# Optimization experiments

Measured on AMD Instinct MI355X. Metric: run time of the kernel, lower is better.

## Reference

```python
import jax, jax.numpy as jnp
import numpy as np

B, T, H, NPRED = 256, 512, 512, 128


def setup_inputs() -> dict:
    key = jax.random.key(0)
    ks = jax.random.split(key, 16)
    s = 1.0 / np.sqrt(H)
    u = lambda k, shape: jax.random.uniform(k, shape, jnp.float32, -s, s)
    return {
        "x": jax.random.normal(ks[0], (B, T), jnp.float32),
        # PyTorch LSTM params, gate order (i, f, g, o); bias = b_ih + b_hh fused
        "enc_Wih0": u(ks[1], (4 * H, 1)),
        "enc_Whh0": u(ks[2], (4 * H, H)),
        "enc_b0": u(ks[3], (4 * H,)),
        "enc_Wih1": u(ks[4], (4 * H, H)),
        "enc_Whh1": u(ks[5], (4 * H, H)),
        "enc_b1": u(ks[6], (4 * H,)),
        "dec_Wih0": u(ks[7], (4 * H, 1)),
        "dec_Whh0": u(ks[8], (4 * H, H)),
        "dec_b0": u(ks[9], (4 * H,)),
        "dec_Wih1": u(ks[10], (4 * H, H)),
        "dec_Whh1": u(ks[11], (4 * H, H)),
        "dec_b1": u(ks[12], (4 * H,)),
        "lin_W": u(ks[13], (H,)),
        "lin_b": u(ks[14], ()),
        "num_predictions": NPRED,
    }


def _cell(xp, h, c, Whh):
    # xp: x @ Wih.T + b (precomputed), shape [B, 4H]
    g = xp + h @ Whh.T
    i, f, gg, o = jnp.split(g, 4, axis=-1)
    c2 = jax.nn.sigmoid(f) * c + jax.nn.sigmoid(i) * jnp.tanh(gg)
    h2 = jax.nn.sigmoid(o) * jnp.tanh(c2)
    return h2, c2


def _lstm_layer(xs, Wih, Whh, b):
    # xs: [B, T, D] -> outputs [B, T, H], final (h, c) each [B, H]
    xp = jnp.einsum('btd,gd->btg', xs, Wih) + b  # input projection for all steps
    Bb = xs.shape[0]
    h0 = jnp.zeros((Bb, Whh.shape[1]), xs.dtype)
    c0 = jnp.zeros_like(h0)

    def step(carry, xt):
        h, c = carry
        h2, c2 = _cell(xt, h, c, Whh)
        return (h2, c2), h2

    (hT, cT), hs = jax.lax.scan(step, (h0, c0), jnp.swapaxes(xp, 0, 1))
    return jnp.swapaxes(hs, 0, 1), hT, cT


def reference(x, enc_Wih0, enc_Whh0, enc_b0, enc_Wih1, enc_Whh1, enc_b1,
              dec_Wih0, dec_Whh0, dec_b0, dec_Wih1, dec_Whh1, dec_b1,
              lin_W, lin_b, num_predictions):
    # Encoder: 2-layer LSTM over the full sequence (encode() feeds [B,T,1] once)
    h_l0, e_h0, e_c0 = _lstm_layer(x[:, :, None], enc_Wih0, enc_Whh0, enc_b0)
    _, e_h1, e_c1 = _lstm_layer(h_l0, enc_Wih1, enc_Whh1, enc_b1)

    def dec_step(carry, _):
        h0, c0, h1, c1, prev = carry
        xp0 = prev[:, None] @ dec_Wih0.T + dec_b0  # [B, 4H]
        h0n, c0n = _cell(xp0, h0, c0, dec_Whh0)
        xp1 = h0n @ dec_Wih1.T + dec_b1
        h1n, c1n = _cell(xp1, h1, c1, dec_Whh1)
        pred = h1n @ lin_W + lin_b  # [B]
        return (h0n, c0n, h1n, c1n, pred), pred

    carry0 = (e_h0, e_c0, e_h1, e_c1, x[:, -1])
    _, preds = jax.lax.scan(dec_step, carry0, None, length=num_predictions)
    return jnp.swapaxes(preds, 0, 1)  # [B, num_predictions]
```

## Files before the change

### kernel.cpp

```cpp
#include <hip/hip_runtime.h>

#define Hh 512
#define Bb 256
#define Tt 512
#define NPR 128
#define BH (Bb*Hh)
#define WN (4*Hh*Hh)
#define LDSB (131072 + 256)

typedef __attribute__((ext_vector_type(8))) short bf8;
typedef __attribute__((ext_vector_type(4))) float f4;
typedef __attribute__((ext_vector_type(4))) unsigned u4;

#define MF(A,B,C) C = __builtin_amdgcn_mfma_f32_16x16x32_bf16(A,B,C,0,0,0)
#define ALD(p)    __hip_atomic_load((p),  __ATOMIC_RELAXED, __HIP_MEMORY_SCOPE_AGENT)
#define AST(p,v)  __hip_atomic_store((p), (v), __ATOMIC_RELAXED, __HIP_MEMORY_SCOPE_AGENT)

__device__ __forceinline__ void ld16(u4& d, const u4* p) {
  asm volatile("global_load_dwordx4 %0, %1, off sc0 sc1" : "=&v"(d) : "v"(p));
}
__device__ __forceinline__ void st16(u4* p, u4 d) {
  asm volatile("global_store_dwordx4 %0, %1, off sc0 sc1" :: "v"(p), "v"(d) : "memory");
}
__device__ __forceinline__ bf8 asbf8(u4 v) {
  union { u4 u; bf8 b; } c; c.u = v; return c.b;
}
#define VW16 { asm volatile("s_waitcnt vmcnt(16)" ::: "memory"); __builtin_amdgcn_sched_barrier(0); }
#define VW0  { asm volatile("s_waitcnt vmcnt(0)"  ::: "memory"); __builtin_amdgcn_sched_barrier(0); }

__device__ __forceinline__ unsigned short f2bf(float x) {
  unsigned u = __float_as_uint(x);
  return (unsigned short)((u + 0x7FFFu + ((u >> 16) & 1u)) >> 16);
}
__device__ __forceinline__ float bf2f(unsigned short h) {
  return __uint_as_float((unsigned)h << 16);
}

__device__ __forceinline__ float sigm(float x) {
  return __builtin_amdgcn_rcpf(1.f + __expf(-x));
}
__device__ __forceinline__ float tanh_f(float x) {
  x = fminf(15.f, fmaxf(-15.f, x));
  const float e = __expf(2.f * x);
  return (e - 1.f) * __builtin_amdgcn_rcpf(e + 1.f);
}

__device__ __forceinline__ u4 pack8(unsigned short v, int lane) {
  unsigned x = v;
  unsigned p1 = (unsigned)__shfl_xor((int)x, 1, 64);
  unsigned u  = (lane & 1) ? ((p1 & 0xFFFFu) | (x << 16)) : ((x & 0xFFFFu) | (p1 << 16));
  unsigned p2 = (unsigned)__shfl_xor((int)u, 2, 64);
  unsigned d0 = (lane & 2) ? p2 : u;
  unsigned d1 = (lane & 2) ? u  : p2;
  unsigned q0 = (unsigned)__shfl_xor((int)d0, 4, 64);
  unsigned q1 = (unsigned)__shfl_xor((int)d1, 4, 64);
  u4 r;
  if (lane & 4) { r[0] = q0; r[1] = q1; r[2] = d0; r[3] = d1; }
  else          { r[0] = d0; r[1] = d1; r[2] = q0; r[3] = q1; }
  return r;
}

struct KP {
  const float *x, *eb0, *eb1, *db0, *db1, *eWih0, *dWih0, *linW, *linb;
  const unsigned short *eWhh0h,*eWhh0l,*eWih1h,*eWih1l,*eWhh1h,*eWhh1l;
  const unsigned short *dWhh0h,*dWhh0l,*dWih1h,*dWih1l,*dWhh1h,*dWhh1l;
  u4 *h0h0,*h0h1,*h0l0,*h0l1,*h1h0,*h1h1,*h1l0,*h1l1;
  float *c0,*c1,*pred,*out;
  unsigned *bar;
};

__device__ void gsync(unsigned* bar, unsigned rnd) {
  asm volatile("s_waitcnt vmcnt(0)" ::: "memory");
  __syncthreads();
  if (threadIdx.x == 0) {
    const int grp = blockIdx.x >> 4;
    unsigned* garr  = bar + grp*32;
    unsigned* cctr  = bar + 512;
    unsigned* cflag = bar + 576;
    const unsigned a = __hip_atomic_fetch_add(garr, 1u, __ATOMIC_RELAXED, __HIP_MEMORY_SCOPE_AGENT);
    if (a == rnd*16u + 15u) {
      const unsigned r = __hip_atomic_fetch_add(cctr, 1u, __ATOMIC_RELAXED, __HIP_MEMORY_SCOPE_AGENT);
      if (r == rnd*16u + 15u) AST(cflag, rnd + 1u);
    }
    while (ALD(cflag) <= rnd) __builtin_amdgcn_s_sleep(2);
  }
  __syncthreads();
  asm volatile("" ::: "memory");
}

__device__ void stageA_w(const unsigned short* Wh, const unsigned short* Wl, int j0, char* L) {
  const int t = threadIdx.x;
  const int r = t >> 2, q = t & 3;
  const int n = (r >> 4)*Hh + j0 + (r & 15);
  const unsigned short* gh = Wh + (size_t)n*Hh;
  const unsigned short* gl = Wl + (size_t)n*Hh;
  char* rowp = L + r*1024;
  #pragma unroll
  for (int u = 0; u < 16; ++u) {
    const int s = q*16 + u;
    const int so = (s ^ (r & 7)) * 16;
    *(uint4*)(rowp + so)         = *(const uint4*)(gh + s*8);
    *(uint4*)(rowp + 65536 + so) = *(const uint4*)(gl + s*8);
  }
  __syncthreads();
}
__device__ void stageB_w(const unsigned short* Wh, const unsigned short* Wl, int j0, char* slab) {
  const int t = threadIdx.x;
  const int r = t >> 3, q = t & 7;
  const int n = (r >> 3)*Hh + j0 + (r & 7);
  const unsigned short* gh = Wh + (size_t)n*Hh;
  const unsigned short* gl = Wl + (size_t)n*Hh;
  char* rowp = slab + r*1024;
  #pragma unroll
  for (int u = 0; u < 8; ++u) {
    const int s = q*8 + u;
    const int so = (s ^ (r & 7)) * 16;
    *(uint4*)(rowp + so)         = *(const uint4*)(gh + s*8);
    *(uint4*)(rowp + 32768 + so) = *(const uint4*)(gl + s*8);
  }
  __syncthreads();
}

__device__ __forceinline__ void stepA(const KP& kp, const char* L, float* sS,
    int m0, int j0, int jg,
    const u4* Ah, const u4* Al,
    const float* sW, const float* bias, float* cst,
    u4* Ho, u4* Lo,
    int smode, int sarg)
{
  const int tid = threadIdx.x;
  if (smode == 0) {
    if (tid < 64) sS[tid] = kp.x[(size_t)(m0 + tid)*Tt + sarg];
  } else {
    const int bl = tid >> 2, part = tid & 3;
    const int b = m0 + bl;
    float a = 0.f;
    #pragma unroll
    for (int u = 0; u < 16; ++u)
      a += ALD(&kp.pred[(part*16 + u)*Bb + b]);
    a += __shfl_xor(a, 1, 64);
    a += __shfl_xor(a, 2, 64);
    const float s = a + kp.linb[0];
    if (part == 0) {
      sS[bl] = s;
      if (jg == 0 && sarg >= 1) kp.out[(size_t)b*NPR + (sarg - 1)] = s;
    }
  }
  __syncthreads();

  const int wv = tid >> 6, lane = tid & 63;
  const int r15 = lane & 15, kg = lane >> 4;
  const int bb = m0 + wv*16 + r15;
  const u4* pAh = Ah + kg*256 + bb;
  const u4* pAl = Al + kg*256 + bb;
  f4 acc[4];
  #pragma unroll
  for (int g = 0; g < 4; ++g) acc[g] = (f4){0.f,0.f,0.f,0.f};
  const int swz = r15 & 7;

  u4 vh[16], vl[16];
  #pragma unroll
  for (int q = 0; q < 16; ++q) {
    ld16(vh[q], pAh + q*1024);
    ld16(vl[q], pAl + q*1024);
  }
  VW16;
  #pragma unroll
  for (int q = 0; q < 8; ++q) {
    const int so = ((q*4 + kg) ^ swz) * 16;
    const bf8 a_h = asbf8(vh[q]), a_l = asbf8(vl[q]);
    #pragma unroll
    for (int g = 0; g < 4; ++g) {
      const int ro = (g*16 + r15)*1024 + so;
      const bf8 w_h = *(const bf8*)(L + ro);
      const bf8 w_l = *(const bf8*)(L + 65536 + ro);
      MF(a_h, w_h, acc[g]); MF(a_l, w_h, acc[g]); MF(a_h, w_l, acc[g]);
    }
  }
  VW0;
  #pragma unroll
  for (int q = 8; q < 16; ++q) {
    const int so = ((q*4 + kg) ^ swz) * 16;
    const bf8 a_h = asbf8(vh[q]), a_l = asbf8(vl[q]);
    #pragma unroll
    for (int g = 0; g < 4; ++g) {
      const int ro = (g*16 + r15)*1024 + so;
      const bf8 w_h = *(const bf8*)(L + ro);
      const bf8 w_l = *(const bf8*)(L + 65536 + ro);
      MF(a_h, w_h, acc[g]); MF(a_l, w_h, acc[g]); MF(a_h, w_l, acc[g]);
    }
  }

  const int j = j0 + r15;
  const float sw0 = sW[j], sw1 = sW[Hh+j], sw2 = sW[2*Hh+j], sw3 = sW[3*Hh+j];
  const float bi = bias[j], bfv = bias[Hh+j], bgv = bias[2*Hh+j], bo = bias[3*Hh+j];
  const int kcA = jg*2 + (r15 >> 3);
  #pragma unroll
  for (int r = 0; r < 4; ++r) {
    const int bloc = wv*16 + kg*4 + r;
    const float sv = sS[bloc];
    const size_t idx = (size_t)(m0 + bloc)*Hh + j;
    const float gi = acc[0][r] + bi  + sv*sw0;
    const float gf = acc[1][r] + bfv + sv*sw1;
    const float gg = acc[2][r] + bgv + sv*sw2;
    const float go = acc[3][r] + bo  + sv*sw3;
    const float c2 = sigm(gf) * cst[idx] + sigm(gi) * tanh_f(gg);
    const float h2 = sigm(go) * tanh_f(c2);
    cst[idx] = c2;
    const unsigned short hh2 = f2bf(h2);
    const unsigned short ll2 = f2bf(h2 - bf2f(hh2));
    const u4 ph = pack8(hh2, lane);
    const u4 pl = pack8(ll2, lane);
    const int slot = kcA*256 + (m0 + wv*16 + kg*4 + r);
    if ((r15 & 7) == 0) { st16(Ho + slot, ph); st16(Lo + slot, pl); }
  }
}

__device__ __forceinline__ void stepB_gemm(const char* Wslab,
    const u4* Ah, const u4* Al, int m0, f4 acc[2][2])
{
  const int tid = threadIdx.x, wv = tid >> 6, lane = tid & 63;
  const int r15 = lane & 15, kg = lane >> 4;
  const int swz = r15 & 7;
  const char* Wh = Wslab;
  const char* Wl = Wslab + 32768;
  #pragma unroll
  for (int mr = 0; mr < 2; ++mr) {
    const int bb = m0 + wv*32 + mr*16 + r15;
    const u4* pAh = Ah + kg*256 + bb;
    const u4* pAl = Al + kg*256 + bb;
    u4 vh[16], vl[16];
    #pragma unroll
    for (int q = 0; q < 16; ++q) {
      ld16(vh[q], pAh + q*1024);
      ld16(vl[q], pAl + q*1024);
    }
    VW16;
    #pragma unroll
    for (int q = 0; q < 8; ++q) {
      const int so = ((q*4 + kg) ^ swz) * 16;
      const bf8 a_h = asbf8(vh[q]), a_l = asbf8(vl[q]);
      const bf8 w0h = *(const bf8*)(Wh + r15*1024 + so);
      const bf8 w1h = *(const bf8*)(Wh + (16 + r15)*1024 + so);
      const bf8 w0l = *(const bf8*)(Wl + r15*1024 + so);
      const bf8 w1l = *(const bf8*)(Wl + (16 + r15)*1024 + so);
      MF(a_h, w0h, acc[mr][0]); MF(a_l, w0h, acc[mr][0]); MF(a_h, w0l, acc[mr][0]);
      MF(a_h, w1h, acc[mr][1]); MF(a_l, w1h, acc[mr][1]); MF(a_h, w1l, acc[mr][1]);
    }
    VW0;
    #pragma unroll
    for (int q = 8; q < 16; ++q) {
      const int so = ((q*4 + kg) ^ swz) * 16;
      const bf8 a_h = asbf8(vh[q]), a_l = asbf8(vl[q]);
      const bf8 w0h = *(const bf8*)(Wh + r15*1024 + so);
      const bf8 w1h = *(const bf8*)(Wh + (16 + r15)*1024 + so);
      const bf8 w0l = *(const bf8*)(Wl + r15*1024 + so);
      const bf8 w1l = *(const bf8*)(Wl + (16 + r15)*1024 + so);
      MF(a_h, w0h, acc[mr][0]); MF(a_l, w0h, acc[mr][0]); MF(a_h, w0l, acc[mr][0]);
      MF(a_h, w1h, acc[mr][1]); MF(a_l, w1h, acc[mr][1]); MF(a_h, w1l, acc[mr][1]);
    }
  }
}

__device__ __forceinline__ void stepB_fin(const KP& kp, int m0, int j0, int jg,
    f4 acc[2][2], const float* bias, float* cst, u4* Ho, u4* Lo, int doPred)
{
  const int tid = threadIdx.x, wv = tid >> 6, lane = tid & 63;
  const int r15 = lane & 15, kg = lane >> 4;
  float og[2][2][4];
  #pragma unroll
  for (int m = 0; m < 2; ++m)
    #pragma unroll
    for (int t = 0; t < 2; ++t)
      #pragma unroll
      for (int c = 0; c < 4; ++c)
        og[m][t][c] = __shfl_xor(acc[m][t][c], 8, 64);
  const int bit = r15 >> 3;
  float gv[4][4];
  #pragma unroll
  for (int g = 0; g < 4; ++g)
    #pragma unroll
    for (int c = 0; c < 4; ++c) {
      const float mine = bit ? acc[1][g>>1][c] : acc[0][g>>1][c];
      const float oth  = bit ? og[1][g>>1][c]  : og[0][g>>1][c];
      gv[g][c] = ((g & 1) == bit) ? mine : oth;
    }
  const int j = j0 + (r15 & 7);
  const float bi = bias[j], bfv = bias[Hh+j], bgv = bias[2*Hh+j], bo = bias[3*Hh+j];
  float hs[4];
  #pragma unroll
  for (int r = 0; r < 4; ++r) {
    const int bl = wv*32 + bit*16 + kg*4 + r;
    const size_t idx = (size_t)(m0 + bl)*Hh + j;
    const float gi = gv[0][r] + bi;
    const float gf = gv[1][r] + bfv;
    const float gg = gv[2][r] + bgv;
    const float go = gv[3][r] + bo;
    const float c2 = sigm(gf) * cst[idx] + sigm(gi) * tanh_f(gg);
    const float h2 = sigm(go) * tanh_f(c2);
    cst[idx] = c2;
    const unsigned short hh2 = f2bf(h2);
    const unsigned short ll2 = f2bf(h2 - bf2f(hh2));
    const u4 ph = pack8(hh2, lane);
    const u4 pl = pack8(ll2, lane);
    const int slot = jg*256 + (m0 + wv*32 + bit*16 + kg*4 + r);
    if ((r15 & 7) == 0) { st16(Ho + slot, ph); st16(Lo + slot, pl); }
    hs[r] = h2;
  }
  if (doPred) {
    const float lw = kp.linW[j];
    #pragma unroll
    for (int r = 0; r < 4; ++r) {
      float p = hs[r] * lw;
      p += __shfl_xor(p, 1, 64);
      p += __shfl_xor(p, 2, 64);
      p += __shfl_xor(p, 4, 64);
      if ((r15 & 7) == 0)
        AST(&kp.pred[jg*Bb + (m0 + wv*32 + bit*16 + kg*4 + r)], p);
    }
  }
}

#define PH0(p) ((p) ? kp.h0h1 : kp.h0h0)
#define PL0(p) ((p) ? kp.h0l1 : kp.h0l0)
#define PH1(p) ((p) ? kp.h1h1 : kp.h1h0)
#define PL1(p) ((p) ? kp.h1l1 : kp.h1l0)

__global__ __launch_bounds__(256, 1) void lstm_persist(KP kp) {
  extern __shared__ char L[];
  float* sS = (float*)(L + 131072);
  const int blk = blockIdx.x;
  const bool roleA = blk < 128;
  int m0, j0, jg;
  if (roleA) { jg = blk >> 2; m0 = (blk & 3) * 64; j0 = jg * 16; }
  else { const int b2 = blk - 128; jg = b2 >> 1; m0 = (b2 & 1) * 128; j0 = jg * 8; }

  if (roleA) stageA_w(kp.eWhh0h, kp.eWhh0l, j0, L);
  else { stageB_w(kp.eWih1h, kp.eWih1l, j0, L); stageB_w(kp.eWhh1h, kp.eWhh1l, j0, L + 65536); }

  unsigned rnd = 0;

  for (int s = 0; s <= Tt; ++s) {
    if (roleA) {
      if (s < Tt)
        stepA(kp, L, sS, m0, j0, jg, PH0(s&1), PL0(s&1), kp.eWih0, kp.eb0,
              kp.c0, PH0((s+1)&1), PL0((s+1)&1), 0, s);
    } else {
      if (s >= 1) {
        f4 acc[2][2];
        acc[0][0] = acc[0][1] = acc[1][0] = acc[1][1] = (f4){0.f,0.f,0.f,0.f};
        stepB_gemm(L,         PH0(s&1),     PL0(s&1),     m0, acc);
        stepB_gemm(L + 65536, PH1((s-1)&1), PL1((s-1)&1), m0, acc);
        stepB_fin(kp, m0, j0, jg, acc, kp.eb1, kp.c1, PH1(s&1), PL1(s&1), 0);
      }
    }
    gsync(kp.bar, rnd++);
  }

  if (roleA) stageA_w(kp.dWhh0h, kp.dWhh0l, j0, L);
  else { stageB_w(kp.dWih1h, kp.dWih1l, j0, L); stageB_w(kp.dWhh1h, kp.dWhh1l, j0, L + 65536); }

  for (int i = 0; i < NPR; ++i) {
    f4 acc[2][2];
    acc[0][0] = acc[0][1] = acc[1][0] = acc[1][1] = (f4){0.f,0.f,0.f,0.f};
    if (roleA) {
      if (i == 0)
        stepA(kp, L, sS, m0, j0, jg, PH0(0), PL0(0), kp.dWih0, kp.db0,
              kp.c0, PH0(1), PL0(1), 0, Tt - 1);
      else
        stepA(kp, L, sS, m0, j0, jg, PH0(i&1), PL0(i&1), kp.dWih0, kp.db0,
              kp.c0, PH0((i+1)&1), PL0((i+1)&1), 1, i);
    } else {
      stepB_gemm(L + 65536, PH1(i&1), PL1(i&1), m0, acc);
    }
    gsync(kp.bar, rnd++);
    if (!roleA) {
      stepB_gemm(L, PH0((i+1)&1), PL0((i+1)&1), m0, acc);
      stepB_fin(kp, m0, j0, jg, acc, kp.db1, kp.c1, PH1((i+1)&1), PL1((i+1)&1), 1);
    }
    gsync(kp.bar, rnd++);
  }

  if (roleA && jg == 0) {
    const int tid = threadIdx.x, bl = tid >> 2, part = tid & 3, b = m0 + bl;
    float a = 0.f;
    #pragma unroll
    for (int u = 0; u < 16; ++u) a += ALD(&kp.pred[(part*16 + u)*Bb + b]);
    a += __shfl_xor(a, 1, 64);
    a += __shfl_xor(a, 2, 64);
    if (part == 0) kp.out[(size_t)b*NPR + 127] = a + kp.linb[0];
  }
}

__global__ __launch_bounds__(256) void conv_w(const float* __restrict__ src,
                                              unsigned short* __restrict__ hi,
                                              unsigned short* __restrict__ lo) {
  const int i = (blockIdx.x * 256 + threadIdx.x) * 4;
  const float4 v = *(const float4*)(src + i);
  const unsigned short h0 = f2bf(v.x), h1 = f2bf(v.y), h2 = f2bf(v.z), h3 = f2bf(v.w);
  ushort4 hv; hv.x = h0; hv.y = h1; hv.z = h2; hv.w = h3;
  ushort4 lv;
  lv.x = f2bf(v.x - bf2f(h0)); lv.y = f2bf(v.y - bf2f(h1));
  lv.z = f2bf(v.z - bf2f(h2)); lv.w = f2bf(v.w - bf2f(h3));
  *(ushort4*)(hi + i) = hv;
  *(ushort4*)(lo + i) = lv;
}

extern "C" void kernel_launch(void* const* d_in, const int* in_sizes, int n_in,
                              void* d_out, int out_size, void* d_ws, size_t ws_size,
                              hipStream_t stream) {
  const float* x     = (const float*)d_in[0];
  const float* eWih0 = (const float*)d_in[1];
  const float* eWhh0 = (const float*)d_in[2];
  const float* eb0   = (const float*)d_in[3];
  const float* eWih1 = (const float*)d_in[4];
  const float* eWhh1 = (const float*)d_in[5];
  const float* eb1   = (const float*)d_in[6];
  const float* dWih0 = (const float*)d_in[7];
  const float* dWhh0 = (const float*)d_in[8];
  const float* db0   = (const float*)d_in[9];
  const float* dWih1 = (const float*)d_in[10];
  const float* dWhh1 = (const float*)d_in[11];
  const float* db1   = (const float*)d_in[12];
  const float* linW  = (const float*)d_in[13];
  const float* linb  = (const float*)d_in[14];
  float* out = (float*)d_out;

  unsigned short* wb = (unsigned short*)d_ws;
  unsigned short* W[12];
  for (int k = 0; k < 12; ++k) W[k] = wb + (size_t)k*WN;
  unsigned short* sb = wb + (size_t)12*WN;
  float* cb   = (float*)(sb + (size_t)8*BH);
  float* c0   = cb;
  float* c1   = cb + BH;
  float* pred = cb + 2*(size_t)BH;
  unsigned* bar = (unsigned*)(pred + 64*Bb);

  (void)hipMemsetAsync(sb + 0*(size_t)BH, 0, (size_t)BH*2, stream);
  (void)hipMemsetAsync(sb + 2*(size_t)BH, 0, (size_t)BH*2, stream);
  (void)hipMemsetAsync(sb + 4*(size_t)BH, 0, (size_t)BH*2, stream);
  (void)hipMemsetAsync(sb + 6*(size_t)BH, 0, (size_t)BH*2, stream);
  (void)hipMemsetAsync(c0, 0, (size_t)BH*4, stream);
  (void)hipMemsetAsync(c1, 0, (size_t)BH*4, stream);
  (void)hipMemsetAsync(bar, 0, 4096, stream);

  conv_w<<<1024, 256, 0, stream>>>(eWhh0, W[0], W[1]);
  conv_w<<<1024, 256, 0, stream>>>(eWih1, W[2], W[3]);
  conv_w<<<1024, 256, 0, stream>>>(eWhh1, W[4], W[5]);
  conv_w<<<1024, 256, 0, stream>>>(dWhh0, W[6], W[7]);
  conv_w<<<1024, 256, 0, stream>>>(dWih1, W[8], W[9]);
  conv_w<<<1024, 256, 0, stream>>>(dWhh1, W[10], W[11]);

  KP kp;
  kp.x = x; kp.eb0 = eb0; kp.eb1 = eb1; kp.db0 = db0; kp.db1 = db1;
  kp.eWih0 = eWih0; kp.dWih0 = dWih0; kp.linW = linW; kp.linb = linb;
  kp.eWhh0h = W[0]; kp.eWhh0l = W[1];
  kp.eWih1h = W[2]; kp.eWih1l = W[3];
  kp.eWhh1h = W[4]; kp.eWhh1l = W[5];
  kp.dWhh0h = W[6]; kp.dWhh0l = W[7];
  kp.dWih1h = W[8]; kp.dWih1l = W[9];
  kp.dWhh1h = W[10]; kp.dWhh1l = W[11];
  kp.h0h0 = (u4*)(sb + 0*(size_t)BH); kp.h0h1 = (u4*)(sb + 1*(size_t)BH);
  kp.h0l0 = (u4*)(sb + 2*(size_t)BH); kp.h0l1 = (u4*)(sb + 3*(size_t)BH);
  kp.h1h0 = (u4*)(sb + 4*(size_t)BH); kp.h1h1 = (u4*)(sb + 5*(size_t)BH);
  kp.h1l0 = (u4*)(sb + 6*(size_t)BH); kp.h1l1 = (u4*)(sb + 7*(size_t)BH);
  kp.c0 = c0; kp.c1 = c1; kp.pred = pred; kp.out = out; kp.bar = bar;

  (void)hipFuncSetAttribute((const void*)lstm_persist,
                            hipFuncAttributeMaxDynamicSharedMemorySize, LDSB);
  void* kargs[] = { (void*)&kp };
  hipError_t rc = hipLaunchCooperativeKernel((const void*)lstm_persist, dim3(256), dim3(256),
                                             kargs, LDSB, stream);
  if (rc != hipSuccess) {
    lstm_persist<<<dim3(256), dim3(256), LDSB, stream>>>(kp);
  }
  (void)in_sizes; (void)n_in; (void)out_size; (void)ws_size;
}
```

Baseline: 10.15 ms.

## Double block size to 512 threads and flatten grid barrier to single counter

The persistent LSTM kernel now runs 512 threads per block. Role-B blocks split their batch rows across 8 waves of 16 rows each instead of 4 waves of 32. Role-A blocks return early from the extra waves, and the weight staging loops are re-split over the larger thread count. The two-level grid barrier becomes one global atomic counter with a shorter sleep, cutting barrier latency at the risk of more contention on a single address. More waves raise register pressure and leave the extra waves idle in role-A blocks.

```diff
diff --git a/kernel.cpp b/kernel.cpp
--- a/kernel.cpp
+++ b/kernel.cpp
@@ -73,16 +73,11 @@
   asm volatile("s_waitcnt vmcnt(0)" ::: "memory");
   __syncthreads();
   if (threadIdx.x == 0) {
-    const int grp = blockIdx.x >> 4;
-    unsigned* garr  = bar + grp*32;
-    unsigned* cctr  = bar + 512;
-    unsigned* cflag = bar + 576;
-    const unsigned a = __hip_atomic_fetch_add(garr, 1u, __ATOMIC_RELAXED, __HIP_MEMORY_SCOPE_AGENT);
-    if (a == rnd*16u + 15u) {
-      const unsigned r = __hip_atomic_fetch_add(cctr, 1u, __ATOMIC_RELAXED, __HIP_MEMORY_SCOPE_AGENT);
-      if (r == rnd*16u + 15u) AST(cflag, rnd + 1u);
-    }
-    while (ALD(cflag) <= rnd) __builtin_amdgcn_s_sleep(2);
+    unsigned* ctr  = bar;
+    unsigned* flag = bar + 64;
+    const unsigned a = __hip_atomic_fetch_add(ctr, 1u, __ATOMIC_RELAXED, __HIP_MEMORY_SCOPE_AGENT);
+    if (a == rnd*256u + 255u) AST(flag, rnd + 1u);
+    while (ALD(flag) <= rnd) __builtin_amdgcn_s_sleep(1);
   }
   __syncthreads();
   asm volatile("" ::: "memory");
@@ -90,14 +85,14 @@
 
 __device__ void stageA_w(const unsigned short* Wh, const unsigned short* Wl, int j0, char* L) {
   const int t = threadIdx.x;
-  const int r = t >> 2, q = t & 3;
+  const int r = t >> 3, q = t & 7;
   const int n = (r >> 4)*Hh + j0 + (r & 15);
   const unsigned short* gh = Wh + (size_t)n*Hh;
   const unsigned short* gl = Wl + (size_t)n*Hh;
   char* rowp = L + r*1024;
   #pragma unroll
-  for (int u = 0; u < 16; ++u) {
-    const int s = q*16 + u;
+  for (int u = 0; u < 8; ++u) {
+    const int s = q*8 + u;
     const int so = (s ^ (r & 7)) * 16;
     *(uint4*)(rowp + so)         = *(const uint4*)(gh + s*8);
     *(uint4*)(rowp + 65536 + so) = *(const uint4*)(gl + s*8);
@@ -106,14 +101,14 @@
 }
 __device__ void stageB_w(const unsigned short* Wh, const unsigned short* Wl, int j0, char* slab) {
   const int t = threadIdx.x;
-  const int r = t >> 3, q = t & 7;
+  const int r = t >> 4, q = t & 15;
   const int n = (r >> 3)*Hh + j0 + (r & 7);
   const unsigned short* gh = Wh + (size_t)n*Hh;
   const unsigned short* gl = Wl + (size_t)n*Hh;
   char* rowp = slab + r*1024;
   #pragma unroll
-  for (int u = 0; u < 8; ++u) {
-    const int s = q*8 + u;
+  for (int u = 0; u < 4; ++u) {
+    const int s = q*4 + u;
     const int so = (s ^ (r & 7)) * 16;
     *(uint4*)(rowp + so)         = *(const uint4*)(gh + s*8);
     *(uint4*)(rowp + 32768 + so) = *(const uint4*)(gl + s*8);
@@ -125,13 +120,12 @@
     int m0, int j0, int jg,
     const u4* Ah, const u4* Al,
     const float* sW, const float* bias, float* cst,
-    u4* Ho, u4* Lo,
-    int smode, int sarg)
+    u4* Ho, u4* Lo, int smode, int sarg)
 {
   const int tid = threadIdx.x;
   if (smode == 0) {
     if (tid < 64) sS[tid] = kp.x[(size_t)(m0 + tid)*Tt + sarg];
-  } else {
+  } else if (tid < 256) {
     const int bl = tid >> 2, part = tid & 3;
     const int b = m0 + bl;
     float a = 0.f;
@@ -148,7 +142,9 @@
   }
   __syncthreads();
 
-  const int wv = tid >> 6, lane = tid & 63;
+  const int wv = tid >> 6;
+  if (wv >= 4) return;
+  const int lane = tid & 63;
   const int r15 = lane & 15, kg = lane >> 4;
   const int bb = m0 + wv*16 + r15;
   const u4* pAh = Ah + kg*256 + bb;
@@ -217,94 +213,81 @@
 }
 
 __device__ __forceinline__ void stepB_gemm(const char* Wslab,
-    const u4* Ah, const u4* Al, int m0, f4 acc[2][2])
+    const u4* Ah, const u4* Al, int m0, f4* acc)
 {
   const int tid = threadIdx.x, wv = tid >> 6, lane = tid & 63;
   const int r15 = lane & 15, kg = lane >> 4;
   const int swz = r15 & 7;
   const char* Wh = Wslab;
   const char* Wl = Wslab + 32768;
-  #pragma unroll
-  for (int mr = 0; mr < 2; ++mr) {
-    const int bb = m0 + wv*32 + mr*16 + r15;
-    const u4* pAh = Ah + kg*256 + bb;
-    const u4* pAl = Al + kg*256 + bb;
-    u4 vh[16], vl[16];
-    #pragma unroll
-    for (int q = 0; q < 16; ++q) {
-      ld16(vh[q], pAh + q*1024);
-      ld16(vl[q], pAl + q*1024);
-    }
-    VW16;
-    #pragma unroll
-    for (int q = 0; q < 8; ++q) {
-      const int so = ((q*4 + kg) ^ swz) * 16;
-      const bf8 a_h = asbf8(vh[q]), a_l = asbf8(vl[q]);
-      const bf8 w0h = *(const bf8*)(Wh + r15*1024 + so);
-      const bf8 w1h = *(const bf8*)(Wh + (16 + r15)*1024 + so);
-      const bf8 w0l = *(const bf8*)(Wl + r15*1024 + so);
-      const bf8 w1l = *(const bf8*)(Wl + (16 + r15)*1024 + so);
-      MF(a_h, w0h, acc[mr][0]); MF(a_l, w0h, acc[mr][0]); MF(a_h, w0l, acc[mr][0]);
-      MF(a_h, w1h, acc[mr][1]); MF(a_l, w1h, acc[mr][1]); MF(a_h, w1l, acc[mr][1]);
-    }
-    VW0;
-    #pragma unroll
-    for (int q = 8; q < 16; ++q) {
-      const int so = ((q*4 + kg) ^ swz) * 16;
-      const bf8 a_h = asbf8(vh[q]), a_l = asbf8(vl[q]);
-      const bf8 w0h = *(const bf8*)(Wh + r15*1024 + so);
-      const bf8 w1h = *(const bf8*)(Wh + (16 + r15)*1024 + so);
-      const bf8 w0l = *(const bf8*)(Wl + r15*1024 + so);
-      const bf8 w1l = *(const bf8*)(Wl + (16 + r15)*1024 + so);
-      MF(a_h, w0h, acc[mr][0]); MF(a_l, w0h, acc[mr][0]); MF(a_h, w0l, acc[mr][0]);
-      MF(a_h, w1h, acc[mr][1]); MF(a_l, w1h, acc[mr][1]); MF(a_h, w1l, acc[mr][1]);
-    }
+  const int bb = m0 + wv*16 + r15;
+  const u4* pAh = Ah + kg*256 + bb;
+  const u4* pAl = Al + kg*256 + bb;
+  u4 vh[16], vl[16];
+  #pragma unroll
+  for (int q = 0; q < 16; ++q) {
+    ld16(vh[q], pAh + q*1024);
+    ld16(vl[q], pAl + q*1024);
+  }
+  VW16;
+  #pragma unroll
+  for (int q = 0; q < 8; ++q) {
+    const int so = ((q*4 + kg) ^ swz) * 16;
+    const bf8 a_h = asbf8(vh[q]), a_l = asbf8(vl[q]);
+    const bf8 w0h = *(const bf8*)(Wh + r15*1024 + so);
+    const bf8 w1h = *(const bf8*)(Wh + (16 + r15)*1024 + so);
+    const bf8 w0l = *(const bf8*)(Wl + r15*1024 + so);
+    const bf8 w1l = *(const bf8*)(Wl + (16 + r15)*1024 + so);
+    MF(a_h, w0h, acc[0]); MF(a_l, w0h, acc[0]); MF(a_h, w0l, acc[0]);
+    MF(a_h, w1h, acc[1]); MF(a_l, w1h, acc[1]); MF(a_h, w1l, acc[1]);
+  }
+  VW0;
+  #pragma unroll
+  for (int q = 8; q < 16; ++q) {
+    const int so = ((q*4 + kg) ^ swz) * 16;
+    const bf8 a_h = asbf8(vh[q]), a_l = asbf8(vl[q]);
+    const bf8 w0h = *(const bf8*)(Wh + r15*1024 + so);
+    const bf8 w1h = *(const bf8*)(Wh + (16 + r15)*1024 + so);
+    const bf8 w0l = *(const bf8*)(Wl + r15*1024 + so);
+    const bf8 w1l = *(const bf8*)(Wl + (16 + r15)*1024 + so);
+    MF(a_h, w0h, acc[0]); MF(a_l, w0h, acc[0]); MF(a_h, w0l, acc[0]);
+    MF(a_h, w1h, acc[1]); MF(a_l, w1h, acc[1]); MF(a_h, w1l, acc[1]);
   }
 }
 
 __device__ __forceinline__ void stepB_fin(const KP& kp, int m0, int j0, int jg,
-    f4 acc[2][2], const float* bias, float* cst, u4* Ho, u4* Lo, int doPred)
+    f4* acc, const float* bias, float* cst, u4* Ho, u4* Lo, int doPred)
 {
   const int tid = threadIdx.x, wv = tid >> 6, lane = tid & 63;
   const int r15 = lane & 15, kg = lane >> 4;
-  float og[2][2][4];
-  #pragma unroll
-  for (int m = 0; m < 2; ++m)
-    #pragma unroll
-    for (int t = 0; t < 2; ++t)
-      #pragma unroll
-      for (int c = 0; c < 4; ++c)
-        og[m][t][c] = __shfl_xor(acc[m][t][c], 8, 64);
-  const int bit = r15 >> 3;
-  float gv[4][4];
-  #pragma unroll
-  for (int g = 0; g < 4; ++g)
-    #pragma unroll
-    for (int c = 0; c < 4; ++c) {
-      const float mine = bit ? acc[1][g>>1][c] : acc[0][g>>1][c];
-      const float oth  = bit ? og[1][g>>1][c]  : og[0][g>>1][c];
-      gv[g][c] = ((g & 1) == bit) ? mine : oth;
-    }
+  float og0[4], og1[4];
+  #pragma unroll
+  for (int c = 0; c < 4; ++c) {
+    og0[c] = __shfl_xor(acc[0][c], 8, 64);
+    og1[c] = __shfl_xor(acc[1][c], 8, 64);
+  }
+  const bool own = (r15 < 8);
   const int j = j0 + (r15 & 7);
   const float bi = bias[j], bfv = bias[Hh+j], bgv = bias[2*Hh+j], bo = bias[3*Hh+j];
   float hs[4];
   #pragma unroll
   for (int r = 0; r < 4; ++r) {
-    const int bl = wv*32 + bit*16 + kg*4 + r;
+    const int bl = wv*16 + kg*4 + r;
     const size_t idx = (size_t)(m0 + bl)*Hh + j;
-    const float gi = gv[0][r] + bi;
-    const float gf = gv[1][r] + bfv;
-    const float gg = gv[2][r] + bgv;
-    const float go = gv[3][r] + bo;
-    const float c2 = sigm(gf) * cst[idx] + sigm(gi) * tanh_f(gg);
+    const float gi = acc[0][r] + bi;
+    const float gf = og0[r]    + bfv;
+    const float gg = acc[1][r] + bgv;
+    const float go = og1[r]    + bo;
+    const float cold = own ? cst[idx] : 0.f;
+    const float c2 = sigm(gf) * cold + sigm(gi) * tanh_f(gg);
     const float h2 = sigm(go) * tanh_f(c2);
-    cst[idx] = c2;
+    if (own) cst[idx] = c2;
     const unsigned short hh2 = f2bf(h2);
     const unsigned short ll2 = f2bf(h2 - bf2f(hh2));
     const u4 ph = pack8(hh2, lane);
     const u4 pl = pack8(ll2, lane);
-    const int slot = jg*256 + (m0 + wv*32 + bit*16 + kg*4 + r);
-    if ((r15 & 7) == 0) { st16(Ho + slot, ph); st16(Lo + slot, pl); }
+    const int slot = jg*256 + (m0 + wv*16 + kg*4 + r);
+    if (r15 == 0) { st16(Ho + slot, ph); st16(Lo + slot, pl); }
     hs[r] = h2;
   }
   if (doPred) {
@@ -315,8 +298,8 @@
       p += __shfl_xor(p, 1, 64);
       p += __shfl_xor(p, 2, 64);
       p += __shfl_xor(p, 4, 64);
-      if ((r15 & 7) == 0)
-        AST(&kp.pred[jg*Bb + (m0 + wv*32 + bit*16 + kg*4 + r)], p);
+      if (r15 == 0)
+        AST(&kp.pred[jg*Bb + (m0 + wv*16 + kg*4 + r)], p);
     }
   }
 }
@@ -326,7 +309,7 @@
 #define PH1(p) ((p) ? kp.h1h1 : kp.h1h0)
 #define PL1(p) ((p) ? kp.h1l1 : kp.h1l0)
 
-__global__ __launch_bounds__(256, 1) void lstm_persist(KP kp) {
+__global__ __launch_bounds__(512) void lstm_persist(KP kp) {
   extern __shared__ char L[];
   float* sS = (float*)(L + 131072);
   const int blk = blockIdx.x;
@@ -347,8 +330,7 @@
               kp.c0, PH0((s+1)&1), PL0((s+1)&1), 0, s);
     } else {
       if (s >= 1) {
-        f4 acc[2][2];
-        acc[0][0] = acc[0][1] = acc[1][0] = acc[1][1] = (f4){0.f,0.f,0.f,0.f};
+        f4 acc[2]; acc[0] = acc[1] = (f4){0.f,0.f,0.f,0.f};
         stepB_gemm(L,         PH0(s&1),     PL0(s&1),     m0, acc);
         stepB_gemm(L + 65536, PH1((s-1)&1), PL1((s-1)&1), m0, acc);
         stepB_fin(kp, m0, j0, jg, acc, kp.eb1, kp.c1, PH1(s&1), PL1(s&1), 0);
@@ -361,8 +343,7 @@
   else { stageB_w(kp.dWih1h, kp.dWih1l, j0, L); stageB_w(kp.dWhh1h, kp.dWhh1l, j0, L + 65536); }
 
   for (int i = 0; i < NPR; ++i) {
-    f4 acc[2][2];
-    acc[0][0] = acc[0][1] = acc[1][0] = acc[1][1] = (f4){0.f,0.f,0.f,0.f};
+    f4 acc[2]; acc[0] = acc[1] = (f4){0.f,0.f,0.f,0.f};
     if (roleA) {
       if (i == 0)
         stepA(kp, L, sS, m0, j0, jg, PH0(0), PL0(0), kp.dWih0, kp.db0,
@@ -381,7 +362,7 @@
     gsync(kp.bar, rnd++);
   }
 
-  if (roleA && jg == 0) {
+  if (roleA && jg == 0 && threadIdx.x < 256) {
     const int tid = threadIdx.x, bl = tid >> 2, part = tid & 3, b = m0 + bl;
     float a = 0.f;
     #pragma unroll
@@ -469,10 +450,10 @@
   (void)hipFuncSetAttribute((const void*)lstm_persist,
                             hipFuncAttributeMaxDynamicSharedMemorySize, LDSB);
   void* kargs[] = { (void*)&kp };
-  hipError_t rc = hipLaunchCooperativeKernel((const void*)lstm_persist, dim3(256), dim3(256),
+  hipError_t rc = hipLaunchCooperativeKernel((const void*)lstm_persist, dim3(256), dim3(512),
                                              kargs, LDSB, stream);
   if (rc != hipSuccess) {
-    lstm_persist<<<dim3(256), dim3(256), LDSB, stream>>>(kp);
+    lstm_persist<<<dim3(256), dim3(512), LDSB, stream>>>(kp);
   }
   (void)in_sizes; (void)n_in; (void)out_size; (void)ws_size;
 }
```

After: 9.454 ms. -6.8%, faster.
